# Kernel optimization log

Hardware: AMD Instinct MI355X
Metric: run time of the kernel (lower is better)

## Reference

```python
import jax, jax.numpy as jnp
import numpy as np

B = 1024
N_ATOMS = 51
FLAT = 7 * 7 * 64  # conv output: 84->20->9->7 spatial, 64 channels


def _conv(x, w, b, s):
    # x: NCHW, w: OIHW, VALID padding, stride s
    y = jax.lax.conv_general_dilated(
        x, w, window_strides=(s, s), padding='VALID',
        dimension_numbers=('NCHW', 'OIHW', 'NCHW'))
    return y + b[None, :, None, None]


def setup_inputs() -> dict:
    key = jax.random.key(0)
    ks = jax.random.split(key, 8)

    def w(k, shape, fan_in):
        return jax.random.normal(k, shape, dtype=jnp.float32) / np.float32(np.sqrt(fan_in))

    return {
        'x': jax.random.uniform(ks[0], (B, 4, 84, 84), jnp.float32, 0.0, 256.0),
        'cw1': w(ks[1], (32, 4, 8, 8), 4 * 8 * 8), 'cb1': jnp.zeros((32,), jnp.float32),
        'cw2': w(ks[2], (64, 32, 4, 4), 32 * 4 * 4), 'cb2': jnp.zeros((64,), jnp.float32),
        'cw3': w(ks[3], (64, 64, 3, 3), 64 * 3 * 3), 'cb3': jnp.zeros((64,), jnp.float32),
        'fw1': w(ks[4], (FLAT, 256), FLAT), 'fb1': jnp.zeros((256,), jnp.float32),
        'fw2': w(ks[5], (256, N_ATOMS), 256), 'fb2': jnp.zeros((N_ATOMS,), jnp.float32),
        'z': jnp.linspace(-10.0, 10.0, N_ATOMS).astype(jnp.float32),  # support atoms
        'n_out': 6,
    }


def reference(x, cw1, cb1, cw2, cb2, cw3, cb3, fw1, fb1, fw2, fb2, z, n_out):
    x = x / 256.0
    x = jax.nn.relu(_conv(x, cw1, cb1, 4))  # [B,32,20,20]
    x = jax.nn.relu(_conv(x, cw2, cb2, 2))  # [B,64,9,9]
    x = jax.nn.relu(_conv(x, cw3, cb3, 1))  # [B,64,7,7]
    h = x.reshape(x.shape[0], -1)           # [B,3136]
    h = jax.nn.relu(h @ fw1 + fb1)          # [B,256]
    p = jax.nn.softmax(h @ fw2 + fb2, axis=1)  # [B,n_atoms]
    # Original loop writes fc_layers(x)[i] identically for every action j:
    dist = jnp.broadcast_to(p[:, None, :], (p.shape[0], n_out, p.shape[1]))
    res = jnp.einsum('bna,a->bn', dist, z)  # expected value per action
    return (dist, res)
```

## Files before the change

### kernel.cpp

```cpp
#include <hip/hip_runtime.h>
#include <hip/hip_fp16.h>

#define RL(x) __builtin_amdgcn_readfirstlane(x)

typedef _Float16 f16x8 __attribute__((ext_vector_type(8)));
typedef float    f32x16 __attribute__((ext_vector_type(16)));

__global__ __launch_bounds__(256) void wprep_k(const float* __restrict__ w1,
                                               const float* __restrict__ w2,
                                               const float* __restrict__ w3,
                                               __half* __restrict__ w1h,
                                               __half* __restrict__ w2h,
                                               float* __restrict__ wt3) {
  int i = blockIdx.x * 256 + threadIdx.x;
  if (i < 8192) {
    int kx = i & 7, oc = (i >> 3) & 31, ky = (i >> 8) & 7, ic = i >> 11;
    w1h[i] = __float2half(w1[oc * 256 + ic * 64 + ky * 8 + kx] * 0.00390625f);
  }
  if (i < 32768) {
    int j = i & 7, ln = (i >> 3) & 31, kh = (i >> 8) & 1, ot = (i >> 9) & 1, ic = i >> 10;
    int k = kh * 8 + j, kx = k >> 2, ky = k & 3, oc = ot * 32 + ln;
    w2h[i] = __float2half(w2[oc * 512 + ic * 16 + ky * 4 + kx]);
  }
  if (i < 36864) {
    int o3 = i % 24, o = o3 / 3, kx = o3 - o * 3;
    int r = i / 24, ocg = r & 7, r2 = r >> 3, ky = r2 % 3, ic = r2 / 3;
    wt3[i] = w3[(ocg * 8 + o) * 576 + ic * 9 + ky * 3 + kx];
  }
}

__global__ __launch_bounds__(256, 2) void conv1_k(const float* __restrict__ x,
                                                  const __half* __restrict__ w1h,
                                                  const float* __restrict__ bias,
                                                  __half* __restrict__ out) {
  const int bid = blockIdx.x;
  const int q  = bid % 10;
  const int bt = bid / 10;
  const int tid = threadIdx.x;
  const int lane = tid & 63;
  const int wv   = RL(tid >> 6);
  const int pyl = wv >> 1;
  const int pxq = wv & 1;
  const int kh = lane >> 5;
  const int ln = lane & 31;

  f32x16 acc[10];
#pragma unroll
  for (int px = 0; px < 10; ++px)
#pragma unroll
    for (int r = 0; r < 16; ++r) acc[px][r] = 0.f;

  const float* xb = x + (bt * 32 + ln) * 28224 + (q * 8 + pyl * 4 + kh) * 84 + pxq * 40;

#pragma unroll 1
  for (int ic = 0; ic < 4; ++ic) {
#pragma unroll
    for (int t = 0; t < 4; ++t) {
      f16x8 aw = *(const f16x8*)(w1h + ((ic * 8 + 2 * t + kh) * 32 + ln) * 8);
      const float* rp = xb + ic * 7056 + 2 * t * 84;
#pragma unroll
      for (int px = 0; px < 10; ++px) {
        float4 lo = *(const float4*)(rp + 4 * px);
        float4 hi = *(const float4*)(rp + 4 * px + 4);
        __half2 p0 = __floats2half2_rn(lo.x, lo.y);
        __half2 p1 = __floats2half2_rn(lo.z, lo.w);
        __half2 p2 = __floats2half2_rn(hi.x, hi.y);
        __half2 p3 = __floats2half2_rn(hi.z, hi.w);
        uint4 u = make_uint4(*(unsigned*)&p0, *(unsigned*)&p1,
                             *(unsigned*)&p2, *(unsigned*)&p3);
        f16x8 bx = *(f16x8*)&u;
        acc[px] = __builtin_amdgcn_mfma_f32_32x32x16_f16(aw, bx, acc[px], 0, 0, 0);
      }
    }
  }

  float bv[16];
#pragma unroll
  for (int r = 0; r < 16; ++r)
    bv[r] = bias[(r & 3) + 8 * (r >> 2) + 4 * kh];

  const int pyg = 2 * q + pyl;
  const int bg  = bt * 32 + ln;
#pragma unroll
  for (int px = 0; px < 10; ++px) {
    const int p = pyg * 20 + pxq * 10 + px;
#pragma unroll
    for (int r = 0; r < 16; ++r) {
      const int oc = (r & 3) + 8 * (r >> 2) + 4 * kh;
      float v = acc[px][r] + bv[r];
      out[(oc * 400 + p) * 1024 + bg] = __float2half(v > 0.f ? v : 0.f);
    }
  }
}

__global__ __launch_bounds__(256, 1) void conv2_k(const __half* __restrict__ in,
                                                  const __half* __restrict__ w2h,
                                                  const float* __restrict__ bias,
                                                  __half* __restrict__ out) {
  __shared__ __align__(16) __half sh[2][9216];
  const int bid = blockIdx.x;
  const int opy = bid % 9;
  const int bt  = bid / 9;
  const int bbase = bt * 64;
  const int tid  = threadIdx.x;
  const int lane = tid & 63;
  const int wv   = RL(tid >> 6);
  const int octile = wv & 1;
  const int bsub   = wv >> 1;
  const int kh = lane >> 5;
  const int ln = lane & 31;

  const unsigned short* inu = (const unsigned short*)in;
  const unsigned short* wu  = (const unsigned short*)w2h;

  int roff[5], offA[5];
#pragma unroll
  for (int p = 0; p < 5; ++p) {
    int idx = p * 256 + tid;
    int px = idx >> 6, b = idx & 63;
    roff[p] = px * 1024 + b;
    offA[p] = b * 128 + ((((px >> 1) ^ (b & 7)) << 3) | ((px & 1) << 2));
  }
  const int base0 = (40 * opy) * 1024 + bbase;

  f32x16 acc[9];
#pragma unroll
  for (int ox = 0; ox < 9; ++ox)
#pragma unroll
    for (int r = 0; r < 16; ++r) acc[ox][r] = 0.f;

  ushort4 s0, s1, s2, s3, s4; uint2 sW;

#define C2_LOAD(icv) do {                                                     \
    const unsigned short* ibp = inu + (icv) * 409600 + base0;                 \
    s0 = make_ushort4(ibp[roff[0]], ibp[roff[0]+20480], ibp[roff[0]+40960], ibp[roff[0]+61440]); \
    s1 = make_ushort4(ibp[roff[1]], ibp[roff[1]+20480], ibp[roff[1]+40960], ibp[roff[1]+61440]); \
    s2 = make_ushort4(ibp[roff[2]], ibp[roff[2]+20480], ibp[roff[2]+40960], ibp[roff[2]+61440]); \
    s3 = make_ushort4(ibp[roff[3]], ibp[roff[3]+20480], ibp[roff[3]+40960], ibp[roff[3]+61440]); \
    s4 = make_ushort4(ibp[roff[4]], ibp[roff[4]+20480], ibp[roff[4]+40960], ibp[roff[4]+61440]); \
    sW = *(const uint2*)(wu + (icv) * 1024 + tid * 4);                        \
  } while (0)

#define C2_STORE(buf) do {                                                    \
    *(uint2*)&sh[buf][offA[0]] = make_uint2((unsigned)s0.x | ((unsigned)s0.y << 16), (unsigned)s0.z | ((unsigned)s0.w << 16)); \
    *(uint2*)&sh[buf][offA[1]] = make_uint2((unsigned)s1.x | ((unsigned)s1.y << 16), (unsigned)s1.z | ((unsigned)s1.w << 16)); \
    *(uint2*)&sh[buf][offA[2]] = make_uint2((unsigned)s2.x | ((unsigned)s2.y << 16), (unsigned)s2.z | ((unsigned)s2.w << 16)); \
    *(uint2*)&sh[buf][offA[3]] = make_uint2((unsigned)s3.x | ((unsigned)s3.y << 16), (unsigned)s3.z | ((unsigned)s3.w << 16)); \
    *(uint2*)&sh[buf][offA[4]] = make_uint2((unsigned)s4.x | ((unsigned)s4.y << 16), (unsigned)s4.z | ((unsigned)s4.w << 16)); \
    *(uint2*)&sh[buf][8192 + tid * 4] = sW;                                   \
  } while (0)

  const int offW = 8192 + octile * 512 + kh * 256 + ln * 8;
  const int bloc = bsub * 32 + ln;
  const int bx7  = bloc & 7;
  const int brow = bloc * 128;

  int cur = 0;
  C2_LOAD(0);
#pragma unroll 1
  for (int ic = 0; ic < 32; ++ic) {
    __syncthreads();
    C2_STORE(cur);
    const int icn = ic < 31 ? ic + 1 : 31;
    C2_LOAD(icn);
    __syncthreads();
    f16x8 aw = *(const f16x8*)&sh[cur][offW];
#pragma unroll
    for (int ox = 0; ox < 9; ++ox) {
      f16x8 bx = *(const f16x8*)&sh[cur][brow + (((ox + kh) ^ bx7) << 3)];
      acc[ox] = __builtin_amdgcn_mfma_f32_32x32x16_f16(aw, bx, acc[ox], 0, 0, 0);
    }
    cur ^= 1;
  }
#undef C2_LOAD
#undef C2_STORE

  float bv[16];
#pragma unroll
  for (int r = 0; r < 16; ++r)
    bv[r] = bias[octile * 32 + (r & 3) + 8 * (r >> 2) + 4 * kh];
  const int bout = bbase + bloc;
#pragma unroll
  for (int ox = 0; ox < 9; ++ox) {
#pragma unroll
    for (int r = 0; r < 16; ++r) {
      const int oc = octile * 32 + (r & 3) + 8 * (r >> 2) + 4 * kh;
      float v = acc[ox][r] + bv[r];
      out[(oc * 81 + opy * 9 + ox) * 1024 + bout] = __float2half(v > 0.f ? v : 0.f);
    }
  }
}

__global__ __launch_bounds__(128, 2) void conv3_k(const __half* __restrict__ in,
                                                  const float* __restrict__ wt,
                                                  const float* __restrict__ bias,
                                                  __half* __restrict__ out) {
  const int bid = blockIdx.x;
  const int ocg = (bid >> 3) & 15;
  const int grp = ((bid >> 7) << 3) | (bid & 7);
  const int opy = grp % 7;
  const int bg  = grp / 7;
  const int tid  = threadIdx.x;
  const int lane = tid & 63;
  const int wv   = RL(tid >> 6);

  float acc[4][7];
#pragma unroll
  for (int o = 0; o < 4; ++o)
#pragma unroll
    for (int ox = 0; ox < 7; ++ox) acc[o][ox] = 0.f;

  const __half* ib = in + bg * 64 + lane;
  const int ic0 = wv * 32;

#pragma unroll 1
  for (int ici = 0; ici < 32; ++ici) {
    const int ic = ic0 + ici;
#pragma unroll
    for (int ky = 0; ky < 3; ++ky) {
      const float* wp = wt + ((ic * 3 + ky) * 8 + (ocg >> 1)) * 24 + (ocg & 1) * 12;
      float wk[12];
#pragma unroll
      for (int q = 0; q < 12; ++q) wk[q] = wp[q];
      const __half* rp = ib + (ic * 81 + (opy + ky) * 9) * 1024;
      float iv[9];
#pragma unroll
      for (int q = 0; q < 9; ++q) iv[q] = __half2float(rp[q * 1024]);
#pragma unroll
      for (int o = 0; o < 4; ++o)
#pragma unroll
        for (int ox = 0; ox < 7; ++ox)
#pragma unroll
          for (int kx = 0; kx < 3; ++kx)
            acc[o][ox] = fmaf(iv[ox + kx], wk[o * 3 + kx], acc[o][ox]);
    }
  }

  __shared__ float red[4][7][64];
  if (wv == 1) {
#pragma unroll
    for (int o = 0; o < 4; ++o)
#pragma unroll
      for (int ox = 0; ox < 7; ++ox) red[o][ox][lane] = acc[o][ox];
  }
  __syncthreads();
  if (wv == 0) {
#pragma unroll
    for (int o = 0; o < 4; ++o) {
      const int oc = ocg * 4 + o;
      const float bj = bias[oc];
#pragma unroll
      for (int ox = 0; ox < 7; ++ox) {
        float v = acc[o][ox] + red[o][ox][lane] + bj;
        out[(oc * 49 + opy * 7 + ox) * 1024 + bg * 64 + lane] =
            __float2half(v > 0.f ? v : 0.f);
      }
    }
  }
}

__global__ __launch_bounds__(64, 2) void fc1a_k(const __half* __restrict__ a,
                                                const float* __restrict__ w,
                                                float* __restrict__ part) {
  const int bid = blockIdx.x;
  const int jg  = (bid >> 3) & 15;
  const int grp = ((bid >> 7) << 3) | (bid & 7);
  const int kc  = grp & 15;
  const int bg  = grp >> 4;
  const int lane = threadIdx.x;

  float acc[16];
#pragma unroll
  for (int j = 0; j < 16; ++j) acc[j] = 0.f;

  const __half* ap = a + kc * 196 * 1024 + bg * 64 + lane;
  const float* wp0 = w + kc * 196 * 256 + jg * 16;

#pragma unroll 4
  for (int k = 0; k < 196; ++k) {
    float av = __half2float(ap[k * 1024]);
    const float* wp = wp0 + k * 256;
#pragma unroll
    for (int j = 0; j < 16; ++j) acc[j] = fmaf(av, wp[j], acc[j]);
  }
#pragma unroll
  for (int j = 0; j < 16; ++j)
    part[(kc * 256 + jg * 16 + j) * 1024 + bg * 64 + lane] = acc[j];
}

__global__ __launch_bounds__(256) void fc1b_k(const float* __restrict__ part,
                                              const float* __restrict__ bias,
                                              float* __restrict__ h) {
  int idx = blockIdx.x * 256 + threadIdx.x;
  float s = bias[idx >> 10];
#pragma unroll
  for (int c = 0; c < 16; ++c) s += part[c * 262144 + idx];
  h[idx] = s > 0.f ? s : 0.f;
}

__global__ __launch_bounds__(256) void fc2_k(const float* __restrict__ h,
                                             const float* __restrict__ w,
                                             const float* __restrict__ bias,
                                             const float* __restrict__ z,
                                             float* __restrict__ dist,
                                             float* __restrict__ res) {
  __shared__ float wl[256 * 51];
  const int tid = threadIdx.x;
#pragma unroll
  for (int i = tid; i < 256 * 51; i += 256) wl[i] = w[i];
  __syncthreads();

  const int j   = tid & 63;
  const int b   = blockIdx.x * 4 + RL(tid >> 6);
  const int jc = j < 51 ? j : 50;
  float acc = bias[jc];
#pragma unroll 8
  for (int k = 0; k < 256; ++k)
    acc = fmaf(h[k * 1024 + b], wl[k * 51 + jc], acc);
  float logit = (j < 51) ? acc : -1e30f;
  float m = logit;
#pragma unroll
  for (int o = 32; o > 0; o >>= 1) m = fmaxf(m, __shfl_xor(m, o, 64));
  float e = (j < 51) ? __expf(logit - m) : 0.f;
  float ssum = e;
#pragma unroll
  for (int o = 32; o > 0; o >>= 1) ssum += __shfl_xor(ssum, o, 64);
  float p = e / ssum;
  float zv = (j < 51) ? z[jc] : 0.f;
  float rz = p * zv;
#pragma unroll
  for (int o = 32; o > 0; o >>= 1) rz += __shfl_xor(rz, o, 64);
  if (j < 51) {
    float* db = dist + b * 6 * 51 + j;
#pragma unroll
    for (int n = 0; n < 6; ++n) db[n * 51] = p;
  }
  if (j < 6) res[b * 6 + j] = rz;
}

extern "C" void kernel_launch(void* const* d_in, const int* in_sizes, int n_in,
                              void* d_out, int out_size, void* d_ws, size_t ws_size,
                              hipStream_t stream) {
  const float* x   = (const float*)d_in[0];
  const float* cw1 = (const float*)d_in[1];
  const float* cb1 = (const float*)d_in[2];
  const float* cw2 = (const float*)d_in[3];
  const float* cb2 = (const float*)d_in[4];
  const float* cw3 = (const float*)d_in[5];
  const float* cb3 = (const float*)d_in[6];
  const float* fw1 = (const float*)d_in[7];
  const float* fb1 = (const float*)d_in[8];
  const float* fw2 = (const float*)d_in[9];
  const float* fb2 = (const float*)d_in[10];
  const float* z   = (const float*)d_in[11];

  float* ws = (float*)d_ws;
  __half* c1t = (__half*)(ws + 6553600);
  __half* c2t = (__half*)(ws + 13107200);
  __half* c3t = (__half*)(ws + 15761408);
  float*  pw  = ws;
  float*  h_t = ws + 4194304;

  float*  wt3n = (float*)d_out;
  __half* w1h  = (__half*)((float*)d_out + 36864);
  __half* w2h  = (__half*)((float*)d_out + 45056);

  float* dist = (float*)d_out;
  float* res  = dist + 1024 * 6 * 51;

  wprep_k<<<144, 256, 0, stream>>>(cw1, cw2, cw3, w1h, w2h, wt3n);
  conv1_k<<<320, 256, 0, stream>>>(x, w1h, cb1, c1t);
  conv2_k<<<144, 256, 0, stream>>>(c1t, w2h, cb2, c2t);
  conv3_k<<<1792, 128, 0, stream>>>(c2t, wt3n, cb3, c3t);
  fc1a_k<<<4096, 64, 0, stream>>>(c3t, fw1, pw);
  fc1b_k<<<1024, 256, 0, stream>>>(pw, fb1, h_t);
  fc2_k<<<256, 256, 0, stream>>>(h_t, fw2, fb2, z, dist, res);
}
```

Before: 428.5 us.

## Remap conv1 to one image per block and add separate transpose kernel

conv1 now gives each block one image and lets MFMA lanes span output pixels instead of batch entries. It writes NCHW-style fp16 output, and a new shared-memory transpose kernel rearranges that into the batch-innermost layout conv2 expects. The aim is contiguous per-image input reads and coalesced output stores, plus more blocks (1024 vs 320) for occupancy. The cost is an extra kernel launch and an extra round trip of the conv1 activation through memory, and some wasted MFMA lanes on the last partial pixel tile.

```diff
diff --git a/kernel.cpp b/kernel.cpp
--- a/kernel.cpp
+++ b/kernel.cpp
@@ -33,43 +33,53 @@
                                                   const __half* __restrict__ w1h,
                                                   const float* __restrict__ bias,
                                                   __half* __restrict__ out) {
-  const int bid = blockIdx.x;
-  const int q  = bid % 10;
-  const int bt = bid / 10;
+  const int b = blockIdx.x;
   const int tid = threadIdx.x;
   const int lane = tid & 63;
   const int wv   = RL(tid >> 6);
-  const int pyl = wv >> 1;
-  const int pxq = wv & 1;
   const int kh = lane >> 5;
   const int ln = lane & 31;
-
-  f32x16 acc[10];
-#pragma unroll
-  for (int px = 0; px < 10; ++px)
-#pragma unroll
-    for (int r = 0; r < 16; ++r) acc[px][r] = 0.f;
-
-  const float* xb = x + (bt * 32 + ln) * 28224 + (q * 8 + pyl * 4 + kh) * 84 + pxq * 40;
+  const int nt = (wv == 0) ? 4 : 3;
+
+  int ibs[4], pvv[4];
+#pragma unroll
+  for (int tt = 0; tt < 4; ++tt) {
+    int p = (wv + tt * 4) * 32 + ln;
+    pvv[tt] = (p < 400);
+    if (p > 399) p = 399;
+    int py = p / 20, px = p - py * 20;
+    ibs[tt] = py * 336 + px * 4;
+  }
+
+  f32x16 acc[4];
+#pragma unroll
+  for (int tt = 0; tt < 4; ++tt)
+#pragma unroll
+    for (int r = 0; r < 16; ++r) acc[tt][r] = 0.f;
+
+  const float* xb = x + b * 28224;
 
 #pragma unroll 1
   for (int ic = 0; ic < 4; ++ic) {
 #pragma unroll
     for (int t = 0; t < 4; ++t) {
       f16x8 aw = *(const f16x8*)(w1h + ((ic * 8 + 2 * t + kh) * 32 + ln) * 8);
-      const float* rp = xb + ic * 7056 + 2 * t * 84;
-#pragma unroll
-      for (int px = 0; px < 10; ++px) {
-        float4 lo = *(const float4*)(rp + 4 * px);
-        float4 hi = *(const float4*)(rp + 4 * px + 4);
-        __half2 p0 = __floats2half2_rn(lo.x, lo.y);
-        __half2 p1 = __floats2half2_rn(lo.z, lo.w);
-        __half2 p2 = __floats2half2_rn(hi.x, hi.y);
-        __half2 p3 = __floats2half2_rn(hi.z, hi.w);
-        uint4 u = make_uint4(*(unsigned*)&p0, *(unsigned*)&p1,
-                             *(unsigned*)&p2, *(unsigned*)&p3);
-        f16x8 bx = *(f16x8*)&u;
-        acc[px] = __builtin_amdgcn_mfma_f32_32x32x16_f16(aw, bx, acc[px], 0, 0, 0);
+      const float* rp = xb + ic * 7056 + (2 * t + kh) * 84;
+#pragma unroll
+      for (int tt = 0; tt < 4; ++tt) {
+        if (tt < nt) {
+          const float* ap = rp + ibs[tt];
+          float4 lo = *(const float4*)ap;
+          float4 hi = *(const float4*)(ap + 4);
+          __half2 p0 = __floats2half2_rn(lo.x, lo.y);
+          __half2 p1 = __floats2half2_rn(lo.z, lo.w);
+          __half2 p2 = __floats2half2_rn(hi.x, hi.y);
+          __half2 p3 = __floats2half2_rn(hi.z, hi.w);
+          uint4 u = make_uint4(*(unsigned*)&p0, *(unsigned*)&p1,
+                               *(unsigned*)&p2, *(unsigned*)&p3);
+          f16x8 bx = *(f16x8*)&u;
+          acc[tt] = __builtin_amdgcn_mfma_f32_32x32x16_f16(aw, bx, acc[tt], 0, 0, 0);
+        }
       }
     }
   }
@@ -79,18 +89,34 @@
   for (int r = 0; r < 16; ++r)
     bv[r] = bias[(r & 3) + 8 * (r >> 2) + 4 * kh];
 
-  const int pyg = 2 * q + pyl;
-  const int bg  = bt * 32 + ln;
-#pragma unroll
-  for (int px = 0; px < 10; ++px) {
-    const int p = pyg * 20 + pxq * 10 + px;
-#pragma unroll
-    for (int r = 0; r < 16; ++r) {
-      const int oc = (r & 3) + 8 * (r >> 2) + 4 * kh;
-      float v = acc[px][r] + bv[r];
-      out[(oc * 400 + p) * 1024 + bg] = __float2half(v > 0.f ? v : 0.f);
-    }
-  }
+#pragma unroll
+  for (int tt = 0; tt < 4; ++tt) {
+    if (tt < nt && pvv[tt]) {
+      const int p = (wv + tt * 4) * 32 + ln;
+#pragma unroll
+      for (int r = 0; r < 16; ++r) {
+        const int oc = (r & 3) + 8 * (r >> 2) + 4 * kh;
+        float v = acc[tt][r] + bv[r];
+        out[b * 12800 + oc * 400 + p] = __float2half(v > 0.f ? v : 0.f);
+      }
+    }
+  }
+}
+
+__global__ __launch_bounds__(256) void t1_k(const __half* __restrict__ in,
+                                            __half* __restrict__ out) {
+  __shared__ __half t[64][65];
+  const int kb = blockIdx.x * 64;
+  const int bb = blockIdx.y * 64;
+  const int lane = threadIdx.x & 63;
+  const int ty   = threadIdx.x >> 6;
+#pragma unroll
+  for (int r = ty; r < 64; r += 4)
+    t[r][lane] = in[(bb + r) * 12800 + kb + lane];
+  __syncthreads();
+#pragma unroll
+  for (int r = ty; r < 64; r += 4)
+    out[(kb + r) * 1024 + bb + lane] = t[lane][r];
 }
 
 __global__ __launch_bounds__(256, 1) void conv2_k(const __half* __restrict__ in,
@@ -355,6 +381,7 @@
   const float* z   = (const float*)d_in[11];
 
   float* ws = (float*)d_ws;
+  __half* c1h = (__half*)ws;
   __half* c1t = (__half*)(ws + 6553600);
   __half* c2t = (__half*)(ws + 13107200);
   __half* c3t = (__half*)(ws + 15761408);
@@ -369,7 +396,8 @@
   float* res  = dist + 1024 * 6 * 51;
 
   wprep_k<<<144, 256, 0, stream>>>(cw1, cw2, cw3, w1h, w2h, wt3n);
-  conv1_k<<<320, 256, 0, stream>>>(x, w1h, cb1, c1t);
+  conv1_k<<<1024, 256, 0, stream>>>(x, w1h, cb1, c1h);
+  t1_k<<<dim3(200, 16), 256, 0, stream>>>(c1h, c1t);
   conv2_k<<<144, 256, 0, stream>>>(c1t, w2h, cb2, c2t);
   conv3_k<<<1792, 128, 0, stream>>>(c2t, wt3n, cb3, c3t);
   fc1a_k<<<4096, 64, 0, stream>>>(c3t, fw1, pw);
```

Measured after the change: 395.4 us. 7.7% less time.
